# Performance work log

Measured on AMD Instinct MI355X. Metric: run time of the kernel, lower is better.

## Reference

```python
import jax, jax.numpy as jnp
import numpy as np

VOCAB = 50000
PAD = VOCAB - 1          # self.pad = vocab - 1
EDIM = 128
WFEAT = 128
LABELS = 2
SLOPE = 0.0
B, N = 64, 512


def setup_inputs() -> dict:
    key = jax.random.key(0)
    ks = jax.random.split(key, 8)
    # padded token ids, variable lengths in [N//2, N]
    doc = jax.random.randint(ks[0], (B, N), 0, VOCAB - 1, dtype=jnp.int32)
    lengths = jax.random.randint(ks[1], (B,), N // 2, N + 1)
    doc = jnp.where(jnp.arange(N)[None, :] < lengths[:, None], doc, PAD).astype(jnp.int32)
    emb = jax.random.normal(ks[2], (VOCAB, EDIM), jnp.float32) * 0.1      # nn.Embedding weight
    W = jax.random.normal(ks[3], (EDIM, WFEAT), jnp.float32) * 0.05      # GAT linear
    a_src = jax.random.normal(ks[4], (WFEAT,), jnp.float32) * 0.05        # attention vec (src half)
    a_dst = jax.random.normal(ks[5], (WFEAT,), jnp.float32) * 0.05        # attention vec (dst half)
    Wc = jax.random.normal(ks[6], (WFEAT, LABELS), jnp.float32) * 0.05    # classifier
    bc = jnp.zeros((LABELS,), jnp.float32)
    return {"doc": doc, "emb": emb, "W": W, "a_src": a_src, "a_dst": a_dst, "Wc": Wc, "bc": bc}


def _build_adj(doc):
    # Vectorized replacement of the python loop over (doc==pad).nonzero():
    # for each pad position d: adj[b, d, :, :] = 0 ; adj[b, :, d, :] = -1
    pad = doc == PAD                               # [B, N]
    row = pad[:, :, None]                          # query i padded
    col = pad[:, None, :]                          # key   j padded
    i = jnp.arange(N)[:, None]
    j = jnp.arange(N)[None, :]
    both = jnp.where(j > i, -1.0, 0.0)             # [N, N]
    adj = jnp.where(row & ~col, 0.0,
          jnp.where(col & ~row, -1.0,
          jnp.where(row & col, both, 1.0)))        # [B, N, N]
    return adj


def reference(doc, emb, W, a_src, a_dst, Wc, bc):
    adj = _build_adj(doc)                          # [B, N, N]
    words = emb[doc]                               # [B, N, E]
    # --- GATLayerBatchEnabled (canonical batched GAT) ---
    h = jnp.einsum('bne,ef->bnf', words, W)        # [B, N, F]
    e_src = h @ a_src                              # [B, N]
    e_dst = h @ a_dst                              # [B, N]
    e = jax.nn.leaky_relu(e_src[:, :, None] + e_dst[:, None, :], negative_slope=SLOPE)
    e = jnp.where(adj > 0, e, -1e9)                # mask non-edges / pads
    attention = jax.nn.softmax(e, axis=-1)         # [B, N, N]
    sentence = jax.nn.elu(jnp.einsum('bij,bjf->bif', attention, h))  # [B, N, F]
    # --- pooling + classifier ---
    poolSentence = jnp.mean(sentence, axis=1)      # [B, F]
    label = jax.nn.softmax(poolSentence @ Wc + bc, axis=0)  # softmax over dim=0 per source
    return (poolSentence, attention, sentence, label)
```

## Files before the change

### kernel.cpp

```cpp
#include <hip/hip_runtime.h>

#define NB 64
#define NN 512
#define ED 128
#define NF 128
#define PAD_ID 49999

typedef unsigned short ushort_t;
typedef __attribute__((ext_vector_type(8))) short short8v;
typedef __attribute__((ext_vector_type(4))) float f32x4;

__device__ __forceinline__ unsigned short f2b(float f) {
    unsigned int u = __float_as_uint(f);
    u = (u + 0x7fffu + ((u >> 16) & 1u)) >> 16;
    return (unsigned short)u;
}
__device__ __forceinline__ float b2f(unsigned short h) {
    return __uint_as_float(((unsigned int)h) << 16);
}

__global__ __launch_bounds__(256) void k_h(
    const int* __restrict__ doc, const float* __restrict__ emb,
    const float* __restrict__ W, const float* __restrict__ a_src,
    const float* __restrict__ a_dst, ushort_t* __restrict__ hT,
    float* __restrict__ esrc, float* __restrict__ edst)
{
    __shared__ float wl[64][128];
    const int tid = threadIdx.x;
    const int t0  = blockIdx.x * 64;
    const int b   = t0 >> 9;
    const int tl0 = t0 & (NN - 1);

#pragma unroll
    for (int k = 0; k < 8; ++k) {
        int idx = tid + k * 256;
        int tok = idx >> 5;
        int e4  = (idx & 31) << 2;
        int d   = doc[t0 + tok];
        *(float4*)&wl[tok][e4] = *(const float4*)(emb + (size_t)d * ED + e4);
    }
    __syncthreads();

    const int fg = tid & 31;  const int f0 = fg << 2;
    const int tg = tid >> 5;

    float acc[8][4] = {};
    for (int e = 0; e < 128; e += 4) {
        float4 wr[4];
#pragma unroll
        for (int k = 0; k < 4; ++k)
            wr[k] = *(const float4*)(W + (e + k) * NF + f0);
#pragma unroll
        for (int r = 0; r < 8; ++r) {
            const float4 x = *(const float4*)&wl[tg * 8 + r][e];
            const float xa[4] = {x.x, x.y, x.z, x.w};
#pragma unroll
            for (int k = 0; k < 4; ++k) {
                acc[r][0] = fmaf(xa[k], wr[k].x, acc[r][0]);
                acc[r][1] = fmaf(xa[k], wr[k].y, acc[r][1]);
                acc[r][2] = fmaf(xa[k], wr[k].z, acc[r][2]);
                acc[r][3] = fmaf(xa[k], wr[k].w, acc[r][3]);
            }
        }
    }

    const float4 as = *(const float4*)(a_src + f0);
    const float4 ad = *(const float4*)(a_dst + f0);
#pragma unroll
    for (int r = 0; r < 8; ++r) {
        float es = acc[r][0]*as.x + acc[r][1]*as.y + acc[r][2]*as.z + acc[r][3]*as.w;
        float ed = acc[r][0]*ad.x + acc[r][1]*ad.y + acc[r][2]*ad.z + acc[r][3]*ad.w;
#pragma unroll
        for (int off = 1; off < 32; off <<= 1) {
            es += __shfl_xor(es, off);
            ed += __shfl_xor(ed, off);
        }
        if (fg == 0) {
            esrc[t0 + tg * 8 + r] = es;
            edst[t0 + tg * 8 + r] = ed;
        }
    }

#pragma unroll
    for (int c = 0; c < 4; ++c) {
        union { ushort_t u[8]; uint4 v; } pk;
#pragma unroll
        for (int r = 0; r < 8; ++r) pk.u[r] = f2b(acc[r][c]);
        *(uint4*)(hT + (size_t)b * NF * NN + (size_t)(f0 + c) * NN + tl0 + tg * 8) = pk.v;
    }
}

__global__ __launch_bounds__(256) void k_attn(
    const int* __restrict__ doc, const ushort_t* __restrict__ hT,
    const float* __restrict__ esrc, const float* __restrict__ edst,
    float* __restrict__ out_att, float* __restrict__ out_sent,
    float* __restrict__ pool)
{
    __shared__ float edl[NN];
    __shared__ float pvl[NN];
    __shared__ float esl[64], rvl[64], invl[64];
    __shared__ float pool_l[NF];

    const int tid = threadIdx.x;
    const int b   = blockIdx.y;
    const int i0  = blockIdx.x * 64;

#pragma unroll
    for (int k = 0; k < 2; ++k) {
        int j = tid + k * 256;
        edl[j] = edst[b * NN + j];
        pvl[j] = (doc[b * NN + j] == PAD_ID) ? 0.f : 1.f;
    }
    if (tid < 64) {
        esl[tid] = esrc[b * NN + i0 + tid];
        rvl[tid] = (doc[b * NN + i0 + tid] == PAD_ID) ? 0.f : 1.f;
    }
    if (tid < NF) pool_l[tid] = 0.f;
    __syncthreads();

    const int w    = tid >> 6;
    const int lane = tid & 63;
    const int mr   = lane & 15;
    const int grp  = lane >> 4;
    const int row_l = w * 16 + mr;
    const float es  = esl[row_l];
    const bool  rv  = rvl[row_l] != 0.f;

    float m = -1e30f;
#pragma unroll
    for (int ks = 0; ks < 16; ++ks) {
        const int j0 = ks * 32 + grp * 8;
        const float4 e0 = *(const float4*)&edl[j0], e1 = *(const float4*)&edl[j0 + 4];
        const float4 c0 = *(const float4*)&pvl[j0], c1 = *(const float4*)&pvl[j0 + 4];
        const float xs[8] = {es+e0.x, es+e0.y, es+e0.z, es+e0.w,
                             es+e1.x, es+e1.y, es+e1.z, es+e1.w};
        const float cs[8] = {c0.x, c0.y, c0.z, c0.w, c1.x, c1.y, c1.z, c1.w};
#pragma unroll
        for (int q = 0; q < 8; ++q) {
            const float x = fmaxf(xs[q], 0.f);
            m = fmaxf(m, cs[q] != 0.f ? x : -1e30f);
        }
    }
    m = fmaxf(m, __shfl_xor(m, 16));
    m = fmaxf(m, __shfl_xor(m, 32));

    float s = 0.f;
    unsigned int pb[64];
#pragma unroll
    for (int ks = 0; ks < 16; ++ks) {
        const int j0 = ks * 32 + grp * 8;
        const float4 e0 = *(const float4*)&edl[j0], e1 = *(const float4*)&edl[j0 + 4];
        const float4 c0 = *(const float4*)&pvl[j0], c1 = *(const float4*)&pvl[j0 + 4];
        const float xs[8] = {es+e0.x, es+e0.y, es+e0.z, es+e0.w,
                             es+e1.x, es+e1.y, es+e1.z, es+e1.w};
        const float cs[8] = {c0.x, c0.y, c0.z, c0.w, c1.x, c1.y, c1.z, c1.w};
        float p[8];
#pragma unroll
        for (int q = 0; q < 8; ++q) {
            const float x = fmaxf(xs[q], 0.f);
            p[q] = rv ? (cs[q] != 0.f ? __expf(x - m) : 0.f) : 1.f;
            s += p[q];
        }
#pragma unroll
        for (int q = 0; q < 4; ++q)
            pb[ks * 4 + q] = ((unsigned)f2b(p[2*q+1]) << 16) | (unsigned)f2b(p[2*q]);
    }
    s += __shfl_xor(s, 16);
    s += __shfl_xor(s, 32);
    const float inv = rv ? (1.f / s) : (1.f / 512.f);
    if (grp == 0) invl[row_l] = inv;

    float* arow = out_att + ((size_t)(b * NN + i0 + row_l)) * NN;
#pragma unroll
    for (int ks = 0; ks < 16; ++ks) {
        float4 o0, o1;
        o0.x = b2f((ushort_t)(pb[ks*4+0] & 0xffff)) * inv;
        o0.y = b2f((ushort_t)(pb[ks*4+0] >> 16))    * inv;
        o0.z = b2f((ushort_t)(pb[ks*4+1] & 0xffff)) * inv;
        o0.w = b2f((ushort_t)(pb[ks*4+1] >> 16))    * inv;
        o1.x = b2f((ushort_t)(pb[ks*4+2] & 0xffff)) * inv;
        o1.y = b2f((ushort_t)(pb[ks*4+2] >> 16))    * inv;
        o1.z = b2f((ushort_t)(pb[ks*4+3] & 0xffff)) * inv;
        o1.w = b2f((ushort_t)(pb[ks*4+3] >> 16))    * inv;
        *(float4*)(arow + ks * 32 + grp * 8)     = o0;
        *(float4*)(arow + ks * 32 + grp * 8 + 4) = o1;
    }
    __syncthreads();

    const ushort_t* hTb = hT + (size_t)b * NF * NN;
#pragma unroll
    for (int nt = 0; nt < 8; ++nt) {
        const int n0 = nt * 16;
        f32x4 acc = {0.f, 0.f, 0.f, 0.f};
        const ushort_t* bp = hTb + (size_t)(n0 + mr) * NN + grp * 8;
#pragma unroll
        for (int ks = 0; ks < 16; ++ks) {
            union { unsigned int u[4]; short8v v; } au;
            au.u[0] = pb[ks*4+0]; au.u[1] = pb[ks*4+1];
            au.u[2] = pb[ks*4+2]; au.u[3] = pb[ks*4+3];
            const short8v bv = *(const short8v*)(bp + ks * 32);
            acc = __builtin_amdgcn_mfma_f32_16x16x32_bf16(au.v, bv, acc, 0, 0, 0);
        }
        const int feat = n0 + mr;
        float psum = 0.f;
#pragma unroll
        for (int reg = 0; reg < 4; ++reg) {
            const int rl = w * 16 + grp * 4 + reg;
            float v = acc[reg] * invl[rl];
            v = v > 0.f ? v : expm1f(v);
            out_sent[((size_t)(b * NN + i0 + rl)) * NF + feat] = v;
            psum += v;
        }
        atomicAdd(&pool_l[feat], psum);
    }
    __syncthreads();
    if (tid < NF) atomicAdd(&pool[b * NF + tid], pool_l[tid]);
}

__global__ __launch_bounds__(128) void k_label(
    const float* __restrict__ poolAccum, const float* __restrict__ Wc,
    const float* __restrict__ bc, float* __restrict__ out_pool,
    float* __restrict__ out_label)
{
    const int tid = threadIdx.x;
    for (int i = tid; i < NB * NF / 4; i += 128) {
        float4 v = *(const float4*)(poolAccum + i * 4);
        v.x *= (1.f/512.f); v.y *= (1.f/512.f); v.z *= (1.f/512.f); v.w *= (1.f/512.f);
        *(float4*)(out_pool + i * 4) = v;
    }
    const int b = tid & 63, c = tid >> 6;
    float z = bc[c];
    for (int f = 0; f < NF; ++f)
        z = fmaf(poolAccum[b * NF + f] * (1.f/512.f), Wc[f * 2 + c], z);
    float mz = z;
#pragma unroll
    for (int off = 32; off; off >>= 1) mz = fmaxf(mz, __shfl_xor(mz, off));
    float e = __expf(z - mz);
    float sv = e;
#pragma unroll
    for (int off = 32; off; off >>= 1) sv += __shfl_xor(sv, off);
    out_label[b * 2 + c] = e / sv;
}

extern "C" void kernel_launch(void* const* d_in, const int* in_sizes, int n_in,
                              void* d_out, int out_size, void* d_ws, size_t ws_size,
                              hipStream_t stream)
{
    const int*   doc   = (const int*)d_in[0];
    const float* emb   = (const float*)d_in[1];
    const float* W     = (const float*)d_in[2];
    const float* a_src = (const float*)d_in[3];
    const float* a_dst = (const float*)d_in[4];
    const float* Wc    = (const float*)d_in[5];
    const float* bc    = (const float*)d_in[6];

    float* out       = (float*)d_out;
    float* out_pool  = out;
    float* out_att   = out_pool + NB * NF;
    float* out_sent  = out_att + (size_t)NB * NN * NN;
    float* out_label = out_sent + (size_t)NB * NN * NF;

    char* base = (char*)d_ws;
    ushort_t* hT  = (ushort_t*)base;
    float* esrc   = (float*)(base + (size_t)NB * NF * NN * 2);
    float* edst   = esrc + NB * NN;
    float* pool   = edst + NB * NN;

    hipMemsetAsync(pool, 0, NB * NF * sizeof(float), stream);

    k_h<<<(NB * NN) / 64, 256, 0, stream>>>(doc, emb, W, a_src, a_dst, hT, esrc, edst);

    dim3 g2(NN / 64, NB);
    k_attn<<<g2, 256, 0, stream>>>(doc, hT, esrc, edst, out_att, out_sent, pool);

    k_label<<<1, 128, 0, stream>>>(pool, Wc, bc, out_pool, out_label);
}
```

Baseline: 182.7 us.

## Split attention rows across waves by column and shrink tiles for more blocks

Measured after the change: 193.6 us. +6.0%, slower.

```diff
diff --git a/kernel.cpp b/kernel.cpp
--- a/kernel.cpp
+++ b/kernel.cpp
@@ -25,14 +25,14 @@
     const float* __restrict__ a_dst, ushort_t* __restrict__ hT,
     float* __restrict__ esrc, float* __restrict__ edst)
 {
-    __shared__ float wl[64][128];
+    __shared__ float wl[32][128];
     const int tid = threadIdx.x;
-    const int t0  = blockIdx.x * 64;
+    const int t0  = blockIdx.x * 32;
     const int b   = t0 >> 9;
     const int tl0 = t0 & (NN - 1);
 
 #pragma unroll
-    for (int k = 0; k < 8; ++k) {
+    for (int k = 0; k < 4; ++k) {
         int idx = tid + k * 256;
         int tok = idx >> 5;
         int e4  = (idx & 31) << 2;
@@ -44,15 +44,15 @@
     const int fg = tid & 31;  const int f0 = fg << 2;
     const int tg = tid >> 5;
 
-    float acc[8][4] = {};
+    float acc[4][4] = {};
     for (int e = 0; e < 128; e += 4) {
         float4 wr[4];
 #pragma unroll
         for (int k = 0; k < 4; ++k)
             wr[k] = *(const float4*)(W + (e + k) * NF + f0);
 #pragma unroll
-        for (int r = 0; r < 8; ++r) {
-            const float4 x = *(const float4*)&wl[tg * 8 + r][e];
+        for (int r = 0; r < 4; ++r) {
+            const float4 x = *(const float4*)&wl[tg * 4 + r][e];
             const float xa[4] = {x.x, x.y, x.z, x.w};
 #pragma unroll
             for (int k = 0; k < 4; ++k) {
@@ -67,7 +67,7 @@
     const float4 as = *(const float4*)(a_src + f0);
     const float4 ad = *(const float4*)(a_dst + f0);
 #pragma unroll
-    for (int r = 0; r < 8; ++r) {
+    for (int r = 0; r < 4; ++r) {
         float es = acc[r][0]*as.x + acc[r][1]*as.y + acc[r][2]*as.z + acc[r][3]*as.w;
         float ed = acc[r][0]*ad.x + acc[r][1]*ad.y + acc[r][2]*ad.z + acc[r][3]*ad.w;
 #pragma unroll
@@ -76,103 +76,107 @@
             ed += __shfl_xor(ed, off);
         }
         if (fg == 0) {
-            esrc[t0 + tg * 8 + r] = es;
-            edst[t0 + tg * 8 + r] = ed;
+            esrc[t0 + tg * 4 + r] = es;
+            edst[t0 + tg * 4 + r] = ed;
         }
     }
 
 #pragma unroll
     for (int c = 0; c < 4; ++c) {
-        union { ushort_t u[8]; uint4 v; } pk;
-#pragma unroll
-        for (int r = 0; r < 8; ++r) pk.u[r] = f2b(acc[r][c]);
-        *(uint4*)(hT + (size_t)b * NF * NN + (size_t)(f0 + c) * NN + tl0 + tg * 8) = pk.v;
-    }
-}
-
-__global__ __launch_bounds__(256) void k_attn(
+        union { ushort_t u[4]; uint2 v; } pk;
+#pragma unroll
+        for (int r = 0; r < 4; ++r) pk.u[r] = f2b(acc[r][c]);
+        *(uint2*)(hT + (size_t)b * NF * NN + (size_t)(f0 + c) * NN + tl0 + tg * 4) = pk.v;
+    }
+}
+
+__global__ __launch_bounds__(256, 6) void k_attn(
     const int* __restrict__ doc, const ushort_t* __restrict__ hT,
     const float* __restrict__ esrc, const float* __restrict__ edst,
     float* __restrict__ out_att, float* __restrict__ out_sent,
     float* __restrict__ pool)
 {
     __shared__ float edl[NN];
-    __shared__ float pvl[NN];
-    __shared__ float esl[64], rvl[64], invl[64];
-    __shared__ float pool_l[NF];
+    __shared__ float esl[16], rvl[16], invl[16];
+    __shared__ float mx[4][16], sx[4][16];
+    __shared__ ushort_t p_l[16][520];
 
     const int tid = threadIdx.x;
     const int b   = blockIdx.y;
-    const int i0  = blockIdx.x * 64;
+    const int i0  = blockIdx.x * 16;
 
 #pragma unroll
     for (int k = 0; k < 2; ++k) {
         int j = tid + k * 256;
-        edl[j] = edst[b * NN + j];
-        pvl[j] = (doc[b * NN + j] == PAD_ID) ? 0.f : 1.f;
-    }
-    if (tid < 64) {
+        float ed = edst[b * NN + j];
+        edl[j] = (doc[b * NN + j] == PAD_ID) ? -3e30f : ed;
+    }
+    if (tid < 16) {
         esl[tid] = esrc[b * NN + i0 + tid];
         rvl[tid] = (doc[b * NN + i0 + tid] == PAD_ID) ? 0.f : 1.f;
     }
-    if (tid < NF) pool_l[tid] = 0.f;
     __syncthreads();
 
     const int w    = tid >> 6;
     const int lane = tid & 63;
     const int mr   = lane & 15;
     const int grp  = lane >> 4;
-    const int row_l = w * 16 + mr;
-    const float es  = esl[row_l];
-    const bool  rv  = rvl[row_l] != 0.f;
+    const int c0   = w * 128;
+    const float es = esl[mr];
+    const bool  rv = rvl[mr] != 0.f;
 
     float m = -1e30f;
 #pragma unroll
-    for (int ks = 0; ks < 16; ++ks) {
-        const int j0 = ks * 32 + grp * 8;
+    for (int ks = 0; ks < 4; ++ks) {
+        const int j0 = c0 + ks * 32 + grp * 8;
         const float4 e0 = *(const float4*)&edl[j0], e1 = *(const float4*)&edl[j0 + 4];
-        const float4 c0 = *(const float4*)&pvl[j0], c1 = *(const float4*)&pvl[j0 + 4];
         const float xs[8] = {es+e0.x, es+e0.y, es+e0.z, es+e0.w,
                              es+e1.x, es+e1.y, es+e1.z, es+e1.w};
-        const float cs[8] = {c0.x, c0.y, c0.z, c0.w, c1.x, c1.y, c1.z, c1.w};
-#pragma unroll
-        for (int q = 0; q < 8; ++q) {
-            const float x = fmaxf(xs[q], 0.f);
-            m = fmaxf(m, cs[q] != 0.f ? x : -1e30f);
-        }
+#pragma unroll
+        for (int q = 0; q < 8; ++q)
+            if (xs[q] > -1e20f) m = fmaxf(m, fmaxf(xs[q], 0.f));
     }
     m = fmaxf(m, __shfl_xor(m, 16));
     m = fmaxf(m, __shfl_xor(m, 32));
+    if (lane < 16) mx[w][mr] = m;
+    __syncthreads();
+    m = fmaxf(fmaxf(mx[0][mr], mx[1][mr]), fmaxf(mx[2][mr], mx[3][mr]));
 
     float s = 0.f;
-    unsigned int pb[64];
-#pragma unroll
-    for (int ks = 0; ks < 16; ++ks) {
-        const int j0 = ks * 32 + grp * 8;
+    unsigned int pb[16];
+#pragma unroll
+    for (int ks = 0; ks < 4; ++ks) {
+        const int j0 = c0 + ks * 32 + grp * 8;
         const float4 e0 = *(const float4*)&edl[j0], e1 = *(const float4*)&edl[j0 + 4];
-        const float4 c0 = *(const float4*)&pvl[j0], c1 = *(const float4*)&pvl[j0 + 4];
         const float xs[8] = {es+e0.x, es+e0.y, es+e0.z, es+e0.w,
                              es+e1.x, es+e1.y, es+e1.z, es+e1.w};
-        const float cs[8] = {c0.x, c0.y, c0.z, c0.w, c1.x, c1.y, c1.z, c1.w};
         float p[8];
 #pragma unroll
         for (int q = 0; q < 8; ++q) {
-            const float x = fmaxf(xs[q], 0.f);
-            p[q] = rv ? (cs[q] != 0.f ? __expf(x - m) : 0.f) : 1.f;
-            s += p[q];
-        }
+            float pv;
+            if (rv) pv = (xs[q] > -1e20f) ? __expf(fmaxf(xs[q], 0.f) - m) : 0.f;
+            else    pv = 1.f;
+            p[q] = pv; s += pv;
+        }
+        union { unsigned int u[4]; uint4 v; } pk;
 #pragma unroll
         for (int q = 0; q < 4; ++q)
-            pb[ks * 4 + q] = ((unsigned)f2b(p[2*q+1]) << 16) | (unsigned)f2b(p[2*q]);
+            pk.u[q] = ((unsigned)f2b(p[2*q+1]) << 16) | (unsigned)f2b(p[2*q]);
+        pb[ks*4+0] = pk.u[0]; pb[ks*4+1] = pk.u[1];
+        pb[ks*4+2] = pk.u[2]; pb[ks*4+3] = pk.u[3];
+        *(uint4*)&p_l[mr][j0] = pk.v;
     }
     s += __shfl_xor(s, 16);
     s += __shfl_xor(s, 32);
+    if (lane < 16) sx[w][mr] = s;
+    __syncthreads();
+    s = sx[0][mr] + sx[1][mr] + sx[2][mr] + sx[3][mr];
     const float inv = rv ? (1.f / s) : (1.f / 512.f);
-    if (grp == 0) invl[row_l] = inv;
-
-    float* arow = out_att + ((size_t)(b * NN + i0 + row_l)) * NN;
-#pragma unroll
-    for (int ks = 0; ks < 16; ++ks) {
+    if (w == 0 && lane < 16) invl[mr] = inv;
+
+    float* arow = out_att + ((size_t)(b * NN + i0 + mr)) * NN + c0;
+#pragma unroll
+    for (int ks = 0; ks < 4; ++ks) {
         float4 o0, o1;
         o0.x = b2f((ushort_t)(pb[ks*4+0] & 0xffff)) * inv;
         o0.y = b2f((ushort_t)(pb[ks*4+0] >> 16))    * inv;
@@ -189,32 +193,31 @@
 
     const ushort_t* hTb = hT + (size_t)b * NF * NN;
 #pragma unroll
-    for (int nt = 0; nt < 8; ++nt) {
-        const int n0 = nt * 16;
+    for (int t = 0; t < 2; ++t) {
+        const int n0 = (w * 2 + t) * 16;
         f32x4 acc = {0.f, 0.f, 0.f, 0.f};
         const ushort_t* bp = hTb + (size_t)(n0 + mr) * NN + grp * 8;
+        const ushort_t* ap = &p_l[mr][grp * 8];
 #pragma unroll
         for (int ks = 0; ks < 16; ++ks) {
-            union { unsigned int u[4]; short8v v; } au;
-            au.u[0] = pb[ks*4+0]; au.u[1] = pb[ks*4+1];
-            au.u[2] = pb[ks*4+2]; au.u[3] = pb[ks*4+3];
+            const short8v av = *(const short8v*)(ap + ks * 32);
             const short8v bv = *(const short8v*)(bp + ks * 32);
-            acc = __builtin_amdgcn_mfma_f32_16x16x32_bf16(au.v, bv, acc, 0, 0, 0);
+            acc = __builtin_amdgcn_mfma_f32_16x16x32_bf16(av, bv, acc, 0, 0, 0);
         }
         const int feat = n0 + mr;
         float psum = 0.f;
 #pragma unroll
         for (int reg = 0; reg < 4; ++reg) {
-            const int rl = w * 16 + grp * 4 + reg;
+            const int rl = grp * 4 + reg;
             float v = acc[reg] * invl[rl];
             v = v > 0.f ? v : expm1f(v);
             out_sent[((size_t)(b * NN + i0 + rl)) * NF + feat] = v;
             psum += v;
         }
-        atomicAdd(&pool_l[feat], psum);
-    }
-    __syncthreads();
-    if (tid < NF) atomicAdd(&pool[b * NF + tid], pool_l[tid]);
+        psum += __shfl_xor(psum, 16);
+        psum += __shfl_xor(psum, 32);
+        if (lane < 16) atomicAdd(&pool[b * NF + feat], psum);
+    }
 }
 
 __global__ __launch_bounds__(128) void k_label(
@@ -222,16 +225,28 @@
     const float* __restrict__ bc, float* __restrict__ out_pool,
     float* __restrict__ out_label)
 {
+    __shared__ float wc0[NF], wc1[NF];
     const int tid = threadIdx.x;
+    if (tid < NF) { wc0[tid] = Wc[tid * 2]; wc1[tid] = Wc[tid * 2 + 1]; }
+    __syncthreads();
+
     for (int i = tid; i < NB * NF / 4; i += 128) {
         float4 v = *(const float4*)(poolAccum + i * 4);
         v.x *= (1.f/512.f); v.y *= (1.f/512.f); v.z *= (1.f/512.f); v.w *= (1.f/512.f);
         *(float4*)(out_pool + i * 4) = v;
     }
+
     const int b = tid & 63, c = tid >> 6;
+    const float* pbp = poolAccum + b * NF;
+    const float* wcp = c ? wc1 : wc0;
     float z = bc[c];
-    for (int f = 0; f < NF; ++f)
-        z = fmaf(poolAccum[b * NF + f] * (1.f/512.f), Wc[f * 2 + c], z);
+    for (int f = 0; f < NF; f += 4) {
+        const float4 pv = *(const float4*)(pbp + f);
+        z = fmaf(pv.x * (1.f/512.f), wcp[f + 0], z);
+        z = fmaf(pv.y * (1.f/512.f), wcp[f + 1], z);
+        z = fmaf(pv.z * (1.f/512.f), wcp[f + 2], z);
+        z = fmaf(pv.w * (1.f/512.f), wcp[f + 3], z);
+    }
     float mz = z;
 #pragma unroll
     for (int off = 32; off; off >>= 1) mz = fmaxf(mz, __shfl_xor(mz, off));
@@ -268,9 +283,9 @@
 
     hipMemsetAsync(pool, 0, NB * NF * sizeof(float), stream);
 
-    k_h<<<(NB * NN) / 64, 256, 0, stream>>>(doc, emb, W, a_src, a_dst, hT, esrc, edst);
-
-    dim3 g2(NN / 64, NB);
+    k_h<<<(NB * NN) / 32, 256, 0, stream>>>(doc, emb, W, a_src, a_dst, hT, esrc, edst);
+
+    dim3 g2(NN / 16, NB);
     k_attn<<<g2, 256, 0, stream>>>(doc, hT, esrc, edst, out_att, out_sent, pool);
 
     k_label<<<1, 128, 0, stream>>>(pool, Wc, bc, out_pool, out_label);
```
